# Optimization experiments

Hardware: AMD Instinct MI355X
Metric: run time of the kernel (lower is better)

The kernel has to match this reference:

```python
import jax, jax.numpy as jnp
import numpy as np

V, E, H, B, S = 50000, 300, 512, 32, 400
SENT_STEP = 20

def _seg_matrix(seq_len, step):
    # PyTorch default: boundaries = range(0, S, step), append S-1 if missing.
    bounds = list(range(0, seq_len, step))
    if bounds[-1] != seq_len - 1:
        bounds.append(seq_len - 1)
    seg = np.searchsorted(np.array(bounds), np.arange(seq_len))  # token -> sentence id
    M = np.zeros((seq_len, len(bounds)), np.float32)
    M[np.arange(seq_len), seg] = 1.0
    M /= M.sum(0, keepdims=True)  # column-normalized -> segment MEAN pooling
    return jnp.asarray(M)

SEG_M = _seg_matrix(S, SENT_STEP)  # [S, n_sent] = [400, 21]

def _gru_dir(x_proj, w_hh, b_hh, reverse):
    # x_proj: [B,T,3H] precomputed x @ W_ih^T + b_ih. PyTorch gate order: r, z, n.
    def step(h, xp):
        gh = h @ w_hh.T + b_hh
        xr, xz, xn = jnp.split(xp, 3, axis=-1)
        hr, hz, hn = jnp.split(gh, 3, axis=-1)
        r = jax.nn.sigmoid(xr + hr)
        z = jax.nn.sigmoid(xz + hz)
        n = jnp.tanh(xn + r * hn)
        h2 = (1.0 - z) * n + z * h
        return h2, h2
    h0 = jnp.zeros((x_proj.shape[0], w_hh.shape[1]), x_proj.dtype)
    h_last, outs = jax.lax.scan(step, h0, x_proj.transpose(1, 0, 2), reverse=reverse)
    return h_last, outs.transpose(1, 0, 2)  # [B,H], [B,T,H]

def _bigru(x, wif, whf, bif, bhf, wib, whb, bib, bhb):
    hf, of = _gru_dir(x @ wif.T + bif, whf, bhf, False)
    hb, ob = _gru_dir(x @ wib.T + bib, whb, bhb, True)
    return jnp.concatenate([of, ob], -1), hf, hb

def setup_inputs():
    key = jax.random.key(0)
    ks = jax.random.split(key, 20)
    f = lambda k, shp: jax.random.normal(k, shp, jnp.float32) * 0.1
    return {
        'input_seq': jax.random.randint(ks[0], (B, S), 0, V),
        'emb': f(ks[1], (V, E)),
        'w_ih_wf': f(ks[2], (3 * H, E)), 'w_hh_wf': f(ks[3], (3 * H, H)),
        'b_ih_wf': f(ks[4], (3 * H,)), 'b_hh_wf': f(ks[5], (3 * H,)),
        'w_ih_wb': f(ks[6], (3 * H, E)), 'w_hh_wb': f(ks[7], (3 * H, H)),
        'b_ih_wb': f(ks[8], (3 * H,)), 'b_hh_wb': f(ks[9], (3 * H,)),
        'w_ih_sf': f(ks[10], (3 * H, 2 * H)), 'w_hh_sf': f(ks[11], (3 * H, H)),
        'b_ih_sf': f(ks[12], (3 * H,)), 'b_hh_sf': f(ks[13], (3 * H,)),
        'w_ih_sb': f(ks[14], (3 * H, 2 * H)), 'w_hh_sb': f(ks[15], (3 * H, H)),
        'b_ih_sb': f(ks[16], (3 * H,)), 'b_hh_sb': f(ks[17], (3 * H,)),
        'fc_w': f(ks[18], (H, 2 * H)), 'fc_b': f(ks[19], (H,)),
    }

def reference(input_seq, emb, w_ih_wf, w_hh_wf, b_ih_wf, b_hh_wf,
              w_ih_wb, w_hh_wb, b_ih_wb, b_hh_wb,
              w_ih_sf, w_hh_sf, b_ih_sf, b_hh_sf,
              w_ih_sb, w_hh_sb, b_ih_sb, b_hh_sb, fc_w, fc_b):
    x = emb[input_seq]  # [B,S,E]; dropout is identity in eval mode
    word_out, _, _ = _bigru(x, w_ih_wf, w_hh_wf, b_ih_wf, b_hh_wf,
                            w_ih_wb, w_hh_wb, b_ih_wb, b_hh_wb)  # [B,S,2H]
    # fused ragged segment-mean pooling (replaces the double python loop)
    sent_rep = jnp.einsum('btd,ts->bsd', word_out, SEG_M)  # [B,n_sent,2H]
    sent_out, hf, hb = _bigru(sent_rep, w_ih_sf, w_hh_sf, b_ih_sf, b_hh_sf,
                              w_ih_sb, w_hh_sb, b_ih_sb, b_hh_sb)
    hidden = jnp.concatenate([hf, hb], -1) @ fc_w.T + fc_b  # [B,H]
    return sent_out, hidden
```

## Files before the change

kernel.cpp:

```cpp
#include <hip/hip_runtime.h>
#include <hip/hip_bf16.h>
#include <hip/hip_cooperative_groups.h>

typedef __bf16 bf16;
typedef __bf16 bf16x4 __attribute__((ext_vector_type(4)));
typedef __bf16 bf16x8 __attribute__((ext_vector_type(8)));
typedef float f32x4 __attribute__((ext_vector_type(4)));

static __device__ __forceinline__ bf16 f2b(float x) { return (bf16)x; }
static __device__ __forceinline__ float b2f(bf16 x) { return (float)x; }

static __device__ __forceinline__ f32x4 mfma16(bf16x8 a, bf16x8 b, f32x4 c) {
  return __builtin_amdgcn_mfma_f32_16x16x32_bf16(a, b, c, 0, 0, 0);
}

static __device__ __forceinline__ bf16x8 loadb8_cc(const bf16* p) {
  bf16x8 v;
  asm volatile("global_load_dwordx4 %0, %1, off sc0 sc1" : "=v"(v) : "v"(p) : "memory");
  return v;
}
static __device__ __forceinline__ void storeb8_cc(bf16* p, bf16x8 v) {
  asm volatile("global_store_dwordx4 %0, %1, off sc0 sc1" :: "v"(p), "v"(v) : "memory");
}

__global__ __launch_bounds__(256) void pad_gather_cvt(
    const float* __restrict__ src, bf16* __restrict__ dst,
    const int* __restrict__ seq, int nrows) {
  int row = blockIdx.x * 4 + (threadIdx.x >> 6);
  int lane = threadIdx.x & 63;
  if (row >= nrows) return;
  int srow;
  if (seq) {
    int s = row >> 5, b = row & 31;
    srow = seq[b * 400 + s];
  } else {
    srow = row;
  }
  const float* sp = src + (size_t)srow * 300;
  bf16* dp = dst + (size_t)row * 320;
  for (int i = lane; i < 320; i += 64) dp[i] = (i < 300) ? f2b(sp[i]) : (bf16)0.f;
}

__global__ __launch_bounds__(256) void cvt_f32_bf16(const float* __restrict__ src,
                                                    bf16* __restrict__ dst,
                                                    int n4) {
  int i = blockIdx.x * 256 + threadIdx.x;
  int stride = gridDim.x * 256;
  for (; i < n4; i += stride) {
    float4 v = ((const float4*)src)[i];
    bf16x4 o = {f2b(v.x), f2b(v.y), f2b(v.z), f2b(v.w)};
    *(bf16x4*)(dst + (size_t)i * 4) = o;
  }
}

__global__ __launch_bounds__(256) void gemm_bt_al(const float* __restrict__ A,
                                                  const bf16* __restrict__ W,
                                                  const float* __restrict__ bias,
                                                  float* __restrict__ C,
                                                  int M, int N, int K) {
  __shared__ bf16 AsH[128][72];
  __shared__ bf16 AsL[128][72];
  __shared__ bf16 Ws[128][72];
  const int n0 = blockIdx.x * 128, m0 = blockIdx.y * 128;
  const int tid = threadIdx.x;
  const int wave = tid >> 6, lane = tid & 63;
  const int l15 = lane & 15, lq = lane >> 4;
  const int wm = (wave >> 1) * 64, wn = (wave & 1) * 64;

  f32x4 acc[4][4] = {};

  for (int k0 = 0; k0 < K; k0 += 64) {
    __syncthreads();
#pragma unroll
    for (int i = 0; i < 8; ++i) {
      int c = tid + 256 * i;
      int r = c >> 4, cc = (c & 15) * 4;
      int gr = m0 + r;
      float4 v = {0.f, 0.f, 0.f, 0.f};
      if (gr < M) v = *(const float4*)(A + (size_t)gr * K + k0 + cc);
      float vv[4] = {v.x, v.y, v.z, v.w};
#pragma unroll
      for (int j = 0; j < 4; ++j) {
        bf16 h = f2b(vv[j]);
        AsH[r][cc + j] = h;
        AsL[r][cc + j] = f2b(vv[j] - b2f(h));
      }
    }
#pragma unroll
    for (int i = 0; i < 4; ++i) {
      int c = tid + 256 * i;
      int r = c >> 3, cc = (c & 7) * 8;
      *(bf16x8*)&Ws[r][cc] = *(const bf16x8*)(W + (size_t)(n0 + r) * K + k0 + cc);
    }
    __syncthreads();
#pragma unroll
    for (int ks = 0; ks < 64; ks += 32) {
      bf16x8 afH[4], afL[4], bfr[4];
#pragma unroll
      for (int i = 0; i < 4; ++i) {
        afH[i] = *(const bf16x8*)&AsH[wm + i * 16 + l15][ks + lq * 8];
        afL[i] = *(const bf16x8*)&AsL[wm + i * 16 + l15][ks + lq * 8];
      }
#pragma unroll
      for (int j = 0; j < 4; ++j)
        bfr[j] = *(const bf16x8*)&Ws[wn + j * 16 + l15][ks + lq * 8];
#pragma unroll
      for (int i = 0; i < 4; ++i)
#pragma unroll
        for (int j = 0; j < 4; ++j) {
          acc[i][j] = mfma16(afH[i], bfr[j], acc[i][j]);
          acc[i][j] = mfma16(afL[i], bfr[j], acc[i][j]);
        }
    }
  }

#pragma unroll
  for (int i = 0; i < 4; ++i)
#pragma unroll
    for (int j = 0; j < 4; ++j) {
      int col = n0 + wn + j * 16 + l15;
      float bv = bias[col];
#pragma unroll
      for (int r = 0; r < 4; ++r) {
        int row = m0 + wm + i * 16 + lq * 4 + r;
        if (row < M) C[(size_t)row * N + col] = acc[i][j][r] + bv;
      }
    }
}

__global__ __launch_bounds__(256) void gru_word(
    const float* __restrict__ whhF, const float* __restrict__ whhB,
    const float* __restrict__ bhhF, const float* __restrict__ bhhB,
    const float* __restrict__ bihF, const float* __restrict__ bihB,
    const bf16* __restrict__ wpad,
    const bf16* __restrict__ xpad,
    bf16* __restrict__ hexb,
    unsigned* __restrict__ flags,
    float* __restrict__ srep)
{
  __shared__ bf16 WlH[48][516];
  __shared__ bf16 WlL[48][516];
  __shared__ bf16 Xw[48][324];
  __shared__ float red[2][4][64][4];
  __shared__ __align__(16) bf16 stg[2][32][16];
  const int tid = threadIdx.x;
  const int bx = blockIdx.x;
  const int dir = bx >> 5, nb = bx & 31;
  const int c0 = nb * 16;
  const float* whh = dir ? whhB : whhF;
  const float* bhh = dir ? bhhB : bhhF;
  const float* bih = dir ? bihB : bihF;
  const bf16* wih = wpad + (size_t)dir * 1536 * 320;
  unsigned* flg = flags + dir * 32;

#pragma unroll
  for (int i = 0; i < 24; ++i) {
    int c = tid + 256 * i;
    int r = c >> 7, kc = (c & 127) * 4;
    int gr = ((r >> 4) << 9) + c0 + (r & 15);
    float4 v = *(const float4*)(whh + (size_t)gr * 512 + kc);
    float vv[4] = {v.x, v.y, v.z, v.w};
#pragma unroll
    for (int j = 0; j < 4; ++j) {
      bf16 h = f2b(vv[j]);
      WlH[r][kc + j] = h;
      WlL[r][kc + j] = f2b(vv[j] - b2f(h));
    }
  }
#pragma unroll
  for (int i = 0; i < 8; ++i) {
    int c = tid + 256 * i;
    if (c < 1920) {
      int r = c / 40, ch = (c % 40) * 8;
      int gr = ((r >> 4) << 9) + c0 + (r & 15);
      *(bf16x8*)&Xw[r][ch] = *(const bf16x8*)(wih + (size_t)gr * 320 + ch);
    }
  }
  __syncthreads();

  const int wave = tid >> 6, lane = tid & 63;
  const int kh = wave >> 1;
  const int mh = wave & 1;
  const int m0 = mh * 16;
  const int l15 = lane & 15, lq = lane >> 4;
  const int colg = c0 + l15;
  const int rowq = m0 + lq * 4;
  const int arow = m0 + l15;
  const int nboff = lq >> 1;
  const int coff = (lq & 1) * 8;
  const float bhr = bhh[colg];
  const float bhz = bhh[512 + colg];
  const float bhn = bhh[1024 + colg];
  const float bir = bih[colg];
  const float biz = bih[512 + colg];
  const float bin_ = bih[1024 + colg];

  float pacc0 = 0.f, pacc1 = 0.f, pacc2 = 0.f, pacc3 = 0.f;
  float hp_reg[4] = {0.f, 0.f, 0.f, 0.f};
  bf16* hex_d = hexb + (size_t)dir * 32768 * 2;

  for (int it = 0; it < 400; ++it) {
    const int t = dir ? (399 - it) : it;
    f32x4 accR = {}, accZ = {}, xN = {}, hN = {};

    {
      const bf16* xrow = xpad + (size_t)(t * 32 + arow) * 320;
      const int kb = kh * 160;
#pragma unroll
      for (int k0 = 0; k0 < 160; k0 += 32) {
        const int kk = kb + k0 + lq * 8;
        bf16x8 a = *(const bf16x8*)(xrow + kk);
        accR = mfma16(a, *(const bf16x8*)&Xw[l15][kk], accR);
        accZ = mfma16(a, *(const bf16x8*)&Xw[16 + l15][kk], accZ);
        xN = mfma16(a, *(const bf16x8*)&Xw[32 + l15][kk], xN);
      }
    }

    if (it > 0) {
      if (tid < 32) {
        while (__hip_atomic_load(&flg[tid], __ATOMIC_RELAXED,
                                 __HIP_MEMORY_SCOPE_AGENT) < (unsigned)it)
          __builtin_amdgcn_s_sleep(1);
      }
      __syncthreads();

      const bf16* hb = hex_d + (size_t)((it - 1) & 1) * 32768;
      const int inrow = arow * 16 + coff;
      bf16x8 hiA[8], loA[8];
#pragma unroll
      for (int c = 0; c < 8; ++c) {
        const bf16* ph = hb + (size_t)(kh * 16 + c * 2 + nboff) * 1024 + inrow;
        hiA[c] = loadb8_cc(ph);
        loA[c] = loadb8_cc(ph + 512);
      }
      asm volatile("s_waitcnt vmcnt(0)" ::: "memory");
      __builtin_amdgcn_sched_barrier(0);

#pragma unroll
      for (int c = 0; c < 8; ++c) {
        const int kk = kh * 256 + c * 32 + lq * 8;
        bf16x8 wrh = *(const bf16x8*)&WlH[l15][kk];
        bf16x8 wrl = *(const bf16x8*)&WlL[l15][kk];
        bf16x8 wzh = *(const bf16x8*)&WlH[16 + l15][kk];
        bf16x8 wzl = *(const bf16x8*)&WlL[16 + l15][kk];
        bf16x8 wnh = *(const bf16x8*)&WlH[32 + l15][kk];
        bf16x8 wnl = *(const bf16x8*)&WlL[32 + l15][kk];
        accR = mfma16(hiA[c], wrh, accR);
        accR = mfma16(loA[c], wrh, accR);
        accR = mfma16(hiA[c], wrl, accR);
        accZ = mfma16(hiA[c], wzh, accZ);
        accZ = mfma16(loA[c], wzh, accZ);
        accZ = mfma16(hiA[c], wzl, accZ);
        hN = mfma16(hiA[c], wnh, hN);
        hN = mfma16(loA[c], wnh, hN);
        hN = mfma16(hiA[c], wnl, hN);
      }
    }

    if (kh == 0) {
      *(f32x4*)&red[mh][0][lane][0] = accR;
      *(f32x4*)&red[mh][1][lane][0] = accZ;
      *(f32x4*)&red[mh][2][lane][0] = xN;
      *(f32x4*)&red[mh][3][lane][0] = hN;
    }
    __syncthreads();
    if (kh == 1) {
      accR = accR + *(const f32x4*)&red[mh][0][lane][0];
      accZ = accZ + *(const f32x4*)&red[mh][1][lane][0];
      xN = xN + *(const f32x4*)&red[mh][2][lane][0];
      hN = hN + *(const f32x4*)&red[mh][3][lane][0];

      float h2v[4];
#pragma unroll
      for (int r = 0; r < 4; ++r) {
        int b = rowq + r;
        float rr = 1.f / (1.f + expf(-(accR[r] + bir + bhr)));
        float zz = 1.f / (1.f + expf(-(accZ[r] + biz + bhz)));
        float nn = tanhf(xN[r] + bin_ + rr * (hN[r] + bhn));
        h2v[r] = (1.f - zz) * nn + zz * hp_reg[r];
        hp_reg[r] = h2v[r];
        bf16 hi = f2b(h2v[r]);
        stg[0][b][l15] = hi;
        stg[1][b][l15] = f2b(h2v[r] - b2f(hi));
      }

      int sg = (t == 0) ? 0 : ((t + 19) / 20);
      if (sg > 20) sg = 20;
      float ic = (sg == 0) ? 1.0f : (sg == 20 ? (1.0f / 19.0f) : 0.05f);
      pacc0 += h2v[0] * ic; pacc1 += h2v[1] * ic;
      pacc2 += h2v[2] * ic; pacc3 += h2v[3] * ic;
      bool flush = dir ? (t == 0 || (t % 20) == 1) : ((t % 20) == 0 || t == 399);
      if (flush) {
        float* sp = srep + ((size_t)(sg * 32 + rowq) * 1024) + (dir << 9) + colg;
        sp[0] = pacc0; sp[1024] = pacc1;
        sp[2048] = pacc2; sp[3072] = pacc3;
        pacc0 = pacc1 = pacc2 = pacc3 = 0.f;
      }
    }

    __syncthreads();
    if (tid < 128) {
      bf16* dst = hex_d + (size_t)(it & 1) * 32768 + (size_t)nb * 1024;
      storeb8_cc(dst + tid * 8, ((const bf16x8*)&stg[0][0][0])[tid]);
    }
    asm volatile("s_waitcnt vmcnt(0)" ::: "memory");
    __syncthreads();
    if (tid == 0)
      __hip_atomic_store(&flg[nb], (unsigned)(it + 1), __ATOMIC_RELAXED,
                         __HIP_MEMORY_SCOPE_AGENT);
  }
}

__global__ __launch_bounds__(256) void gru_sent(
    const float* __restrict__ whhF, const float* __restrict__ whhB,
    const float* __restrict__ bhhF, const float* __restrict__ bhhB,
    const float* __restrict__ xproj,
    bf16* __restrict__ hexb,
    unsigned* __restrict__ flags,
    float* __restrict__ out,
    float* __restrict__ hfin)
{
  __shared__ bf16 WlH[48][516];
  __shared__ bf16 WlL[48][516];
  __shared__ float red[2][3][64][4];
  __shared__ __align__(16) bf16 stg[2][32][16];
  const int tid = threadIdx.x;
  const int bx = blockIdx.x;
  const int dir = bx >> 5, nb = bx & 31;
  const int c0 = nb * 16;
  const float* whh = dir ? whhB : whhF;
  const float* bhh = dir ? bhhB : bhhF;
  unsigned* flg = flags + dir * 32;

#pragma unroll
  for (int i = 0; i < 24; ++i) {
    int c = tid + 256 * i;
    int r = c >> 7, kc = (c & 127) * 4;
    int gr = ((r >> 4) << 9) + c0 + (r & 15);
    float4 v = *(const float4*)(whh + (size_t)gr * 512 + kc);
    float vv[4] = {v.x, v.y, v.z, v.w};
#pragma unroll
    for (int j = 0; j < 4; ++j) {
      bf16 h = f2b(vv[j]);
      WlH[r][kc + j] = h;
      WlL[r][kc + j] = f2b(vv[j] - b2f(h));
    }
  }
  __syncthreads();

  const int wave = tid >> 6, lane = tid & 63;
  const int kh = wave >> 1;
  const int mh = wave & 1;
  const int m0 = mh * 16;
  const int l15 = lane & 15, lq = lane >> 4;
  const int colg = c0 + l15;
  const int rowq = m0 + lq * 4;
  const int arow = m0 + l15;
  const int nboff = lq >> 1;
  const int coff = (lq & 1) * 8;
  const float bhr = bhh[colg];
  const float bhz = bhh[512 + colg];
  const float bhn = bhh[1024 + colg];

  float hp_reg[4] = {0.f, 0.f, 0.f, 0.f};
  bf16* hex_d = hexb + (size_t)dir * 32768 * 2;

  for (int it = 0; it < 21; ++it) {
    const int t = dir ? (20 - it) : it;
    f32x4 accR = {}, accZ = {}, hN = {};

    if (it > 0) {
      if (tid < 32) {
        while (__hip_atomic_load(&flg[tid], __ATOMIC_RELAXED,
                                 __HIP_MEMORY_SCOPE_AGENT) < (unsigned)it)
          __builtin_amdgcn_s_sleep(1);
      }
      __syncthreads();

      const bf16* hb = hex_d + (size_t)((it - 1) & 1) * 32768;
      const int inrow = arow * 16 + coff;
      bf16x8 hiA[8], loA[8];
#pragma unroll
      for (int c = 0; c < 8; ++c) {
        const bf16* ph = hb + (size_t)(kh * 16 + c * 2 + nboff) * 1024 + inrow;
        hiA[c] = loadb8_cc(ph);
        loA[c] = loadb8_cc(ph + 512);
      }
      asm volatile("s_waitcnt vmcnt(0)" ::: "memory");
      __builtin_amdgcn_sched_barrier(0);

#pragma unroll
      for (int c = 0; c < 8; ++c) {
        const int kk = kh * 256 + c * 32 + lq * 8;
        bf16x8 wrh = *(const bf16x8*)&WlH[l15][kk];
        bf16x8 wrl = *(const bf16x8*)&WlL[l15][kk];
        bf16x8 wzh = *(const bf16x8*)&WlH[16 + l15][kk];
        bf16x8 wzl = *(const bf16x8*)&WlL[16 + l15][kk];
        bf16x8 wnh = *(const bf16x8*)&WlH[32 + l15][kk];
        bf16x8 wnl = *(const bf16x8*)&WlL[32 + l15][kk];
        accR = mfma16(hiA[c], wrh, accR);
        accR = mfma16(loA[c], wrh, accR);
        accR = mfma16(hiA[c], wrl, accR);
        accZ = mfma16(hiA[c], wzh, accZ);
        accZ = mfma16(loA[c], wzh, accZ);
        accZ = mfma16(hiA[c], wzl, accZ);
        hN = mfma16(hiA[c], wnh, hN);
        hN = mfma16(loA[c], wnh, hN);
        hN = mfma16(hiA[c], wnl, hN);
      }
    }

    if (kh == 0) {
      *(f32x4*)&red[mh][0][lane][0] = accR;
      *(f32x4*)&red[mh][1][lane][0] = accZ;
      *(f32x4*)&red[mh][2][lane][0] = hN;
    }
    __syncthreads();
    if (kh == 1) {
      accR = accR + *(const f32x4*)&red[mh][0][lane][0];
      accZ = accZ + *(const f32x4*)&red[mh][1][lane][0];
      hN = hN + *(const f32x4*)&red[mh][2][lane][0];

      const float* xp = xproj + ((size_t)dir * 672 + t * 32) * 1536;
#pragma unroll
      for (int r = 0; r < 4; ++r) {
        int b = rowq + r;
        float xr = xp[b * 1536 + colg];
        float xz = xp[b * 1536 + 512 + colg];
        float xn = xp[b * 1536 + 1024 + colg];
        float rr = 1.f / (1.f + expf(-(xr + accR[r] + bhr)));
        float zz = 1.f / (1.f + expf(-(xz + accZ[r] + bhz)));
        float nn = tanhf(xn + rr * (hN[r] + bhn));
        float h2 = (1.f - zz) * nn + zz * hp_reg[r];
        hp_reg[r] = h2;
        bf16 hi = f2b(h2);
        stg[0][b][l15] = hi;
        stg[1][b][l15] = f2b(h2 - b2f(hi));
        out[(size_t)b * (21 * 1024) + (size_t)t * 1024 + (dir << 9) + colg] = h2;
        if (it == 20) hfin[(dir << 14) + b * 512 + colg] = h2;
      }
    }

    __syncthreads();
    if (tid < 128) {
      bf16* dst = hex_d + (size_t)(it & 1) * 32768 + (size_t)nb * 1024;
      storeb8_cc(dst + tid * 8, ((const bf16x8*)&stg[0][0][0])[tid]);
    }
    asm volatile("s_waitcnt vmcnt(0)" ::: "memory");
    __syncthreads();
    if (tid == 0)
      __hip_atomic_store(&flg[nb], (unsigned)(it + 1), __ATOMIC_RELAXED,
                         __HIP_MEMORY_SCOPE_AGENT);
  }
}

__global__ __launch_bounds__(256) void fc_k(const float* __restrict__ hfin,
                                            const float* __restrict__ fcw,
                                            const float* __restrict__ fcb,
                                            float* __restrict__ out) {
  __shared__ float hl[1024];
  int b = blockIdx.x, tid = threadIdx.x;
  for (int i = tid; i < 512; i += 256) {
    hl[i] = hfin[b * 512 + i];
    hl[512 + i] = hfin[16384 + b * 512 + i];
  }
  __syncthreads();
  for (int j = tid; j < 512; j += 256) {
    const float* wr = fcw + (size_t)j * 1024;
    float acc = 0.f;
    for (int k = 0; k < 1024; k += 4) {
      float4 wv = *(const float4*)(wr + k);
      acc += hl[k] * wv.x + hl[k + 1] * wv.y + hl[k + 2] * wv.z +
             hl[k + 3] * wv.w;
    }
    out[688128 + b * 512 + j] = acc + fcb[j];
  }
}

extern "C" void kernel_launch(void* const* d_in, const int* in_sizes, int n_in,
                              void* d_out, int out_size, void* d_ws,
                              size_t ws_size, hipStream_t stream) {
  const int* seq = (const int*)d_in[0];
  const float* emb = (const float*)d_in[1];
  const float* w_ih_wf = (const float*)d_in[2];
  const float* w_hh_wf = (const float*)d_in[3];
  const float* b_ih_wf = (const float*)d_in[4];
  const float* b_hh_wf = (const float*)d_in[5];
  const float* w_ih_wb = (const float*)d_in[6];
  const float* w_hh_wb = (const float*)d_in[7];
  const float* b_ih_wb = (const float*)d_in[8];
  const float* b_hh_wb = (const float*)d_in[9];
  const float* w_ih_sf = (const float*)d_in[10];
  const float* w_hh_sf = (const float*)d_in[11];
  const float* b_ih_sf = (const float*)d_in[12];
  const float* b_hh_sf = (const float*)d_in[13];
  const float* w_ih_sb = (const float*)d_in[14];
  const float* w_hh_sb = (const float*)d_in[15];
  const float* b_ih_sb = (const float*)d_in[16];
  const float* b_hh_sb = (const float*)d_in[17];
  const float* fc_w = (const float*)d_in[18];
  const float* fc_b = (const float*)d_in[19];

  char* ws = (char*)d_ws;
  bf16* xpad = (bf16*)(ws + 0);
  bf16* wpadw = (bf16*)(ws + 8192000);
  bf16* wihs = (bf16*)(ws + 10158080);
  float* srep = (float*)(ws + 16449536);
  float* xps = (float*)(ws + 19202048);
  bf16* hexb = (bf16*)(ws + 27459584);
  float* hfin = (float*)(ws + 27721728);
  unsigned* flags = (unsigned*)(ws + 27852800);

  hipMemsetAsync(ws + 16449536, 0, 27854848 - 16449536, stream);

  pad_gather_cvt<<<3200, 256, 0, stream>>>(emb, xpad, seq, 12800);
  pad_gather_cvt<<<384, 256, 0, stream>>>(w_ih_wf, wpadw, nullptr, 1536);
  pad_gather_cvt<<<384, 256, 0, stream>>>(w_ih_wb, wpadw + 1536 * 320, nullptr,
                                          1536);
  cvt_f32_bf16<<<1536, 256, 0, stream>>>(w_ih_sf, wihs, 393216);
  cvt_f32_bf16<<<1536, 256, 0, stream>>>(w_ih_sb, wihs + 1572864, 393216);

  {
    unsigned* flgW = flags;
    void* args[] = {(void*)&w_hh_wf, (void*)&w_hh_wb, (void*)&b_hh_wf,
                    (void*)&b_hh_wb, (void*)&b_ih_wf, (void*)&b_ih_wb,
                    (void*)&wpadw,   (void*)&xpad,    (void*)&hexb,
                    (void*)&flgW,    (void*)&srep};
    hipLaunchCooperativeKernel((const void*)gru_word, dim3(64), dim3(256),
                               args, 0, stream);
  }

  dim3 g2(12, 6);
  gemm_bt_al<<<g2, 256, 0, stream>>>(srep, wihs, b_ih_sf, xps, 672, 1536, 1024);
  gemm_bt_al<<<g2, 256, 0, stream>>>(srep, wihs + 1572864, b_ih_sb,
                                     xps + (size_t)672 * 1536, 672, 1536, 1024);

  {
    unsigned* flgS = flags + 128;
    float* outp = (float*)d_out;
    const float* xpsc = xps;
    void* args[] = {(void*)&w_hh_sf, (void*)&w_hh_sb, (void*)&b_hh_sf,
                    (void*)&b_hh_sb, (void*)&xpsc,    (void*)&hexb,
                    (void*)&flgS,    (void*)&outp,    (void*)&hfin};
    hipLaunchCooperativeKernel((const void*)gru_sent, dim3(64), dim3(256),
                               args, 0, stream);
  }

  fc_k<<<32, 256, 0, stream>>>(hfin, fc_w, fc_b, (float*)d_out);
}
```

Before: 2.309 ms.

## Prefetch next-step input rows and shorten the per-step flag publish path

In the word-level GRU, the x-row operands for the next timestep are now loaded into registers during the current step. The input-projection MFMAs are issued while the hidden-state exchange loads are in flight, which moves their global-load latency off the serial recurrence. The hidden-state store and flag publish are now done by a single wave without a second block-wide barrier, and the spin-wait no longer sleeps, in both the word and sentence kernels. Wave 0 relies on a hand-written vmcnt(5) count to order its stores before the flag write while its prefetches stay outstanding. That count is fragile, and busy-spinning without sleep adds memory polling pressure.

```diff
diff --git a/kernel.cpp b/kernel.cpp
--- a/kernel.cpp
+++ b/kernel.cpp
@@ -188,6 +188,7 @@
   const int arow = m0 + l15;
   const int nboff = lq >> 1;
   const int coff = (lq & 1) * 8;
+  const int kb = kh * 160;
   const float bhr = bhh[colg];
   const float bhz = bhh[512 + colg];
   const float bhn = bhh[1024 + colg];
@@ -199,43 +200,47 @@
   float hp_reg[4] = {0.f, 0.f, 0.f, 0.f};
   bf16* hex_d = hexb + (size_t)dir * 32768 * 2;
 
+  bf16x8 xr[5];
+  {
+    const int t0 = dir ? 399 : 0;
+    const bf16* xrow = xpad + (size_t)(t0 * 32 + arow) * 320;
+#pragma unroll
+    for (int c = 0; c < 5; ++c) xr[c] = *(const bf16x8*)(xrow + kb + c * 32 + lq * 8);
+  }
+
   for (int it = 0; it < 400; ++it) {
     const int t = dir ? (399 - it) : it;
     f32x4 accR = {}, accZ = {}, xN = {}, hN = {};
 
-    {
-      const bf16* xrow = xpad + (size_t)(t * 32 + arow) * 320;
-      const int kb = kh * 160;
-#pragma unroll
-      for (int k0 = 0; k0 < 160; k0 += 32) {
-        const int kk = kb + k0 + lq * 8;
-        bf16x8 a = *(const bf16x8*)(xrow + kk);
-        accR = mfma16(a, *(const bf16x8*)&Xw[l15][kk], accR);
-        accZ = mfma16(a, *(const bf16x8*)&Xw[16 + l15][kk], accZ);
-        xN = mfma16(a, *(const bf16x8*)&Xw[32 + l15][kk], xN);
-      }
-    }
-
+    bf16x8 hiA[8], loA[8];
     if (it > 0) {
       if (tid < 32) {
         while (__hip_atomic_load(&flg[tid], __ATOMIC_RELAXED,
-                                 __HIP_MEMORY_SCOPE_AGENT) < (unsigned)it)
-          __builtin_amdgcn_s_sleep(1);
+                                 __HIP_MEMORY_SCOPE_AGENT) < (unsigned)it) {}
       }
       __syncthreads();
 
       const bf16* hb = hex_d + (size_t)((it - 1) & 1) * 32768;
       const int inrow = arow * 16 + coff;
-      bf16x8 hiA[8], loA[8];
 #pragma unroll
       for (int c = 0; c < 8; ++c) {
         const bf16* ph = hb + (size_t)(kh * 16 + c * 2 + nboff) * 1024 + inrow;
         hiA[c] = loadb8_cc(ph);
         loA[c] = loadb8_cc(ph + 512);
       }
+    }
+
+#pragma unroll
+    for (int c = 0; c < 5; ++c) {
+      const int kk = kb + c * 32 + lq * 8;
+      accR = mfma16(xr[c], *(const bf16x8*)&Xw[l15][kk], accR);
+      accZ = mfma16(xr[c], *(const bf16x8*)&Xw[16 + l15][kk], accZ);
+      xN = mfma16(xr[c], *(const bf16x8*)&Xw[32 + l15][kk], xN);
+    }
+
+    if (it > 0) {
       asm volatile("s_waitcnt vmcnt(0)" ::: "memory");
       __builtin_amdgcn_sched_barrier(0);
-
 #pragma unroll
       for (int c = 0; c < 8; ++c) {
         const int kk = kh * 256 + c * 32 + lq * 8;
@@ -298,16 +303,34 @@
       }
     }
 
+    if (wave != 0 && it < 399) {
+      const int tn = dir ? (399 - (it + 1)) : (it + 1);
+      const bf16* xrow = xpad + (size_t)(tn * 32 + arow) * 320;
+#pragma unroll
+      for (int c = 0; c < 5; ++c)
+        xr[c] = *(const bf16x8*)(xrow + kb + c * 32 + lq * 8);
+    }
+
     __syncthreads();
-    if (tid < 128) {
+
+    if (wave == 0) {
       bf16* dst = hex_d + (size_t)(it & 1) * 32768 + (size_t)nb * 1024;
-      storeb8_cc(dst + tid * 8, ((const bf16x8*)&stg[0][0][0])[tid]);
-    }
-    asm volatile("s_waitcnt vmcnt(0)" ::: "memory");
-    __syncthreads();
-    if (tid == 0)
-      __hip_atomic_store(&flg[nb], (unsigned)(it + 1), __ATOMIC_RELAXED,
-                         __HIP_MEMORY_SCOPE_AGENT);
+      storeb8_cc(dst + lane * 8, ((const bf16x8*)&stg[0][0][0])[lane]);
+      storeb8_cc(dst + (lane + 64) * 8, ((const bf16x8*)&stg[0][0][0])[lane + 64]);
+      if (it < 399) {
+        const int tn = dir ? (399 - (it + 1)) : (it + 1);
+        const bf16* xrow = xpad + (size_t)(tn * 32 + arow) * 320;
+#pragma unroll
+        for (int c = 0; c < 5; ++c)
+          xr[c] = *(const bf16x8*)(xrow + kb + c * 32 + lq * 8);
+        asm volatile("s_waitcnt vmcnt(5)" ::: "memory");
+      } else {
+        asm volatile("s_waitcnt vmcnt(0)" ::: "memory");
+      }
+      if (tid == 0)
+        __hip_atomic_store(&flg[nb], (unsigned)(it + 1), __ATOMIC_RELAXED,
+                           __HIP_MEMORY_SCOPE_AGENT);
+    }
   }
 }
 
@@ -369,17 +392,16 @@
     const int t = dir ? (20 - it) : it;
     f32x4 accR = {}, accZ = {}, hN = {};
 
+    bf16x8 hiA[8], loA[8];
     if (it > 0) {
       if (tid < 32) {
         while (__hip_atomic_load(&flg[tid], __ATOMIC_RELAXED,
-                                 __HIP_MEMORY_SCOPE_AGENT) < (unsigned)it)
-          __builtin_amdgcn_s_sleep(1);
+                                 __HIP_MEMORY_SCOPE_AGENT) < (unsigned)it) {}
       }
       __syncthreads();
 
       const bf16* hb = hex_d + (size_t)((it - 1) & 1) * 32768;
       const int inrow = arow * 16 + coff;
-      bf16x8 hiA[8], loA[8];
 #pragma unroll
       for (int c = 0; c < 8; ++c) {
         const bf16* ph = hb + (size_t)(kh * 16 + c * 2 + nboff) * 1024 + inrow;
@@ -442,15 +464,15 @@
     }
 
     __syncthreads();
-    if (tid < 128) {
+    if (wave == 0) {
       bf16* dst = hex_d + (size_t)(it & 1) * 32768 + (size_t)nb * 1024;
-      storeb8_cc(dst + tid * 8, ((const bf16x8*)&stg[0][0][0])[tid]);
-    }
-    asm volatile("s_waitcnt vmcnt(0)" ::: "memory");
-    __syncthreads();
-    if (tid == 0)
-      __hip_atomic_store(&flg[nb], (unsigned)(it + 1), __ATOMIC_RELAXED,
-                         __HIP_MEMORY_SCOPE_AGENT);
+      storeb8_cc(dst + lane * 8, ((const bf16x8*)&stg[0][0][0])[lane]);
+      storeb8_cc(dst + (lane + 64) * 8, ((const bf16x8*)&stg[0][0][0])[lane + 64]);
+      asm volatile("s_waitcnt vmcnt(0)" ::: "memory");
+      if (tid == 0)
+        __hip_atomic_store(&flg[nb], (unsigned)(it + 1), __ATOMIC_RELAXED,
+                           __HIP_MEMORY_SCOPE_AGENT);
+    }
   }
 }
 
```

New measurement: 2.445 ms. +5.9%, slower.
